# Kernel optimization log

Hardware: AMD Instinct MI355X
Metric: run time of the kernel (lower is better)

Reference implementation:

```python
import jax, jax.numpy as jnp
import numpy as np

H = 64  # hidden_size
B, T1, T2, T3 = 4096, 512, 256, 128


def setup_inputs() -> dict:
    key = jax.random.key(0)
    ks = jax.random.split(key, 18)
    s = 1.0 / np.sqrt(H)  # torch LSTMCell init scale
    def p(k, shape, scale):
        return jax.random.normal(k, shape, dtype=jnp.float32) * scale
    return {
        "x1": p(ks[0], (B, T1), 1.0),
        "x2": p(ks[1], (B, T2), 1.0),
        "x3": p(ks[2], (B, T3), 1.0),
        "W_ih3": p(ks[3], (4 * H, 3), s), "W_hh3": p(ks[4], (4 * H, H), s),
        "b_ih3": p(ks[5], (4 * H,), s), "b_hh3": p(ks[6], (4 * H,), s),
        "W_ih2": p(ks[7], (4 * H, 2), s), "W_hh2": p(ks[8], (4 * H, H), s),
        "b_ih2": p(ks[9], (4 * H,), s), "b_hh2": p(ks[10], (4 * H,), s),
        "W_ih1": p(ks[11], (4 * H, 1), s), "W_hh1": p(ks[12], (4 * H, H), s),
        "b_ih1": p(ks[13], (4 * H,), s), "b_hh1": p(ks[14], (4 * H,), s),
        "W_out": p(ks[15], (1, H), s), "b_out": p(ks[16], (1,), s),
    }


def reference(x1, x2, x3,
              W_ih3, W_hh3, b_ih3, b_hh3,
              W_ih2, W_hh2, b_ih2, b_hh2,
              W_ih1, W_hh1, b_ih1, b_hh1,
              W_out, b_out):
    h = W_hh3.shape[1]
    Bb, t1 = x1.shape
    r2, r3 = t1 // x2.shape[1], t1 // x3.shape[1]
    # Pad input weights to width 3; concat order is [x1, x2, x3] (zeros where absent),
    # so padded-column zeros reproduce the narrower cells exactly.
    Wi = jnp.stack([W_ih3,
                    jnp.pad(W_ih2, ((0, 0), (0, 1))),
                    jnp.pad(W_ih1, ((0, 0), (0, 2)))])  # [3, 4H, 3]
    Wh = jnp.stack([W_hh3, W_hh2, W_hh1])               # [3, 4H, H]
    bs = jnp.stack([b_ih3 + b_hh3, b_ih2 + b_hh2, b_ih1 + b_hh1])  # [3, 4H]
    t = np.arange(t1)
    has2 = (t % r2 == 0)
    has3 = (t % r3 == 0)
    assert not np.any(has3 & ~has2), "ratio2 must divide ratio3 for the concat-order mapping"
    # width 3 -> cell3 (type 0), width 2 -> cell2 (type 1), width 1 -> cell1 (type 2)
    step_type = jnp.asarray(2 - has2.astype(np.int32) - has3.astype(np.int32))
    xs = jnp.zeros((t1, Bb, 3), x1.dtype)
    xs = xs.at[:, :, 0].set(x1.T)
    xs = xs.at[::r2, :, 1].set(x2.T)
    xs = xs.at[::r3, :, 2].set(x3.T)

    def step(carry, inp):
        hx, cx = carry
        x, ty = inp
        g = x @ Wi[ty].T + hx @ Wh[ty].T + bs[ty]  # [B, 4H]
        i, f, gg, o = jnp.split(g, 4, axis=-1)     # torch gate order i,f,g,o
        cx = jax.nn.sigmoid(f) * cx + jax.nn.sigmoid(i) * jnp.tanh(gg)
        hx = jax.nn.sigmoid(o) * jnp.tanh(cx)
        return (hx, cx), None

    z = jnp.zeros((Bb, h), x1.dtype)
    (hx, _), _ = jax.lax.scan(step, (z, z), (xs, step_type))
    return jax.nn.sigmoid(hx @ W_out.T + b_out)  # [B, 1]
```

## Files before the change

### kernel.cpp

```cpp
#include <hip/hip_runtime.h>


typedef __attribute__((ext_vector_type(8))) short short8v;
typedef __attribute__((ext_vector_type(4))) float float4v;
typedef __attribute__((ext_vector_type(2))) float float2v;
typedef __attribute__((ext_vector_type(4))) unsigned int uint4v;
typedef __attribute__((ext_vector_type(2))) unsigned int uint2v;

template <int N> struct IC { static constexpr int value = N; };

#define AST 72

#if __has_builtin(__builtin_amdgcn_exp2f)
#define EXP2F(x) __builtin_amdgcn_exp2f(x)
#else
#define EXP2F(x) exp2f(x)
#endif
#if __has_builtin(__builtin_amdgcn_rcpf)
#define RCPF(x) __builtin_amdgcn_rcpf(x)
#else
#define RCPF(x) (1.0f / (x))
#endif

#define NL2E -1.4426950408889634f
#define NL2E2 -2.8853900817779268f

__device__ __forceinline__ short f2bf(float f) {
  union { float f; unsigned u; } v; v.f = f;
  unsigned r = v.u + 0x7FFFu + ((v.u >> 16) & 1u);
  return (short)(r >> 16);
}
__device__ __forceinline__ float bf2f(short h) {
  union { float f; unsigned u; } v;
  v.u = ((unsigned)(unsigned short)h) << 16;
  return v.f;
}
__device__ __forceinline__ unsigned cvt_pk_bf16(float lo, float hi) {
  unsigned r;
  asm("v_cvt_pk_bf16_f32 %0, %1, %2" : "=v"(r) : "v"(lo), "v"(hi));
  return r;
}
__device__ __forceinline__ unsigned permb(unsigned hi, unsigned lo, unsigned sel) {
#if __has_builtin(__builtin_amdgcn_perm)
  return __builtin_amdgcn_perm(hi, lo, sel);
#else
  union { unsigned u[2]; unsigned char b[8]; } s;
  s.u[0] = lo; s.u[1] = hi;
  unsigned r = 0;
  for (int i = 0; i < 4; ++i) r |= (unsigned)s.b[(sel >> (8 * i)) & 7] << (8 * i);
  return r;
#endif
}
__device__ __forceinline__ float rcp1p(float y) {
  return RCPF(1.0f + EXP2F(y));
}
__device__ __forceinline__ float fsig(float x) { return rcp1p(x * NL2E); }

__global__ __launch_bounds__(256, 1) void mlstm_kernel(
    const float* __restrict__ x1, const float* __restrict__ x2,
    const float* __restrict__ x3,
    const float* __restrict__ Wi3, const float* __restrict__ Wh3,
    const float* __restrict__ bi3, const float* __restrict__ bh3,
    const float* __restrict__ Wi2, const float* __restrict__ Wh2,
    const float* __restrict__ bi2, const float* __restrict__ bh2,
    const float* __restrict__ Wi1, const float* __restrict__ Wh1,
    const float* __restrict__ bi1, const float* __restrict__ bh1,
    const float* __restrict__ Wout, const float* __restrict__ bout,
    float* __restrict__ out) {
  __shared__ __attribute__((aligned(16))) short Ab0[16 * AST];
  __shared__ __attribute__((aligned(16))) short Ab1[16 * AST];

  const int tid = threadIdx.x;
  const int w = tid >> 6;
  const int lane = tid & 63;
  const int q = lane >> 4;
  const int c = lane & 15;
  const int R0 = blockIdx.x << 4;

  for (int idx = tid; idx < 16 * AST; idx += 256) {
    Ab0[idx] = 0;
    Ab1[idx] = 0;
  }

  const float* xr1 = x1 + (size_t)(R0 + c) * 512;
  const float* xr2 = x2 + (size_t)(R0 + c) * 256;
  const float* xr3 = x3 + (size_t)(R0 + c) * 128;

  float4v xf1 = *(const float4v*)(xr1);
  float2v xf2 = *(const float2v*)(xr2);
  float xf3 = xr3[0];

  short8v whs[3][4][2];
  short8v wix[3][4];
  float4v bias4[3][4];
  {
    const float* WhA[3] = {Wh3, Wh2, Wh1};
    const float* WiA[3] = {Wi3, Wi2, Wi1};
    const float* biA[3] = {bi3, bi2, bi1};
    const float* bhA[3] = {bh3, bh2, bh1};
    const int wdt[3] = {3, 2, 1};
#pragma unroll
    for (int ty = 0; ty < 3; ++ty) {
#pragma unroll
      for (int g = 0; g < 4; ++g) {
        const float sg = (g == 2) ? NL2E2 : NL2E;
        const int n = g * 64 + 16 * w + c;
#pragma unroll
        for (int kf = 0; kf < 2; ++kf) {
          short8v v;
#pragma unroll
          for (int j = 0; j < 8; ++j)
            v[j] = f2bf(sg * WhA[ty][n * 64 + kf * 32 + q * 8 + j]);
          whs[ty][g][kf] = v;
        }
        short8v v2 = {0, 0, 0, 0, 0, 0, 0, 0};
        if (q == 0) {
#pragma unroll
          for (int j = 0; j < 3; ++j)
            if (j < wdt[ty]) v2[j] = f2bf(sg * WiA[ty][n * wdt[ty] + j]);
        }
        wix[ty][g] = v2;
        float4v bv;
#pragma unroll
        for (int r = 0; r < 4; ++r) {
          const int nd = g * 64 + 16 * w + 4 * q + r;
          bv[r] = sg * (biA[ty][nd] + bhA[ty][nd]);
        }
        bias4[ty][g] = bv;
      }
    }
  }

  const int afo = c * AST + q * 8;
  const int hwo = c * AST + 16 * w + 4 * q;

  __syncthreads();

  float cx[4] = {0.f, 0.f, 0.f, 0.f};

  unsigned d0, d1, d2, d3, xcw;
  auto cvtgrp = [&]() {
    unsigned pA = cvt_pk_bf16(xf1[0], xf1[1]);
    unsigned pB = cvt_pk_bf16(xf1[2], xf1[3]);
    unsigned p2 = cvt_pk_bf16(xf2[0], xf2[1]);
    xcw = cvt_pk_bf16(xf3, 0.0f);
    d0 = permb(p2, pA, 0x05040100);
    d1 = permb(p2, pA, 0x05040302);
    d2 = permb(p2, pB, 0x07060100);
    d3 = permb(p2, pB, 0x07060302);
  };
  cvtgrp();

  auto stepf = [&](auto tyc, unsigned dS, unsigned dx3, const short* rbuf,
                   short* wbuf) {
    constexpr int TY = decltype(tyc)::value;
    uint4v au = {dS, dx3, 0u, 0u};
    short8v a2 = __builtin_bit_cast(short8v, au);
    short8v a0 = *(const short8v*)(rbuf + afo);
    short8v a1 = *(const short8v*)(rbuf + afo + 32);

    float4v acc[4];
#pragma unroll
    for (int g = 0; g < 4; ++g) {
      float4v z = bias4[TY][g];
      z = __builtin_amdgcn_mfma_f32_16x16x32_bf16(wix[TY][g], a2, z, 0, 0, 0);
      z = __builtin_amdgcn_mfma_f32_16x16x32_bf16(whs[TY][g][0], a0, z, 0, 0, 0);
      z = __builtin_amdgcn_mfma_f32_16x16x32_bf16(whs[TY][g][1], a1, z, 0, 0, 0);
      acc[g] = z;
    }

    float h[4];
#pragma unroll
    for (int r = 0; r < 4; ++r) {
      float e0 = EXP2F(acc[0][r]);
      float e1 = EXP2F(acc[1][r]);
      float e2 = EXP2F(__builtin_fminf(acc[2][r], 60.0f));
      float e3 = EXP2F(acc[3][r]);
      float sitg = (1.0f - e2) * RCPF((1.0f + e0) * (1.0f + e2));
      float ncx = __builtin_fmaf(RCPF(1.0f + e1), cx[r], sitg);
      cx[r] = ncx;
      float e4 = EXP2F(__builtin_fminf(ncx * NL2E2, 60.0f));
      h[r] = (1.0f - e4) * RCPF((1.0f + e3) * (1.0f + e4));
    }
    uint2v pk;
    pk[0] = cvt_pk_bf16(h[0], h[1]);
    pk[1] = cvt_pk_bf16(h[2], h[3]);
    *(uint2v*)(wbuf + hwo) = pk;
    __syncthreads();
  };

  for (int t4 = 0; t4 < 512; t4 += 4) {
    stepf(IC<0>{}, d0, xcw, Ab0, Ab1);
    int tp = (t4 + 4 > 508) ? 508 : (t4 + 4);
    xf1 = *(const float4v*)(xr1 + tp);
    xf2 = *(const float2v*)(xr2 + (tp >> 1));
    xf3 = xr3[tp >> 2];
    stepf(IC<2>{}, d1, xcw, Ab1, Ab0);
    stepf(IC<1>{}, d2, xcw, Ab0, Ab1);
    stepf(IC<2>{}, d3, xcw, Ab1, Ab0);
    cvtgrp();
  }

  if (tid < 16) {
    float s = bout[0];
    const short* hr = Ab0 + tid * AST;
#pragma unroll
    for (int k = 0; k < 64; ++k)
      s = __builtin_fmaf(bf2f(hr[k]), Wout[k], s);
    out[R0 + tid] = fsig(s);
  }
}

extern "C" void kernel_launch(void* const* d_in, const int* in_sizes, int n_in,
                              void* d_out, int out_size, void* d_ws,
                              size_t ws_size, hipStream_t stream) {
  const float* x1 = (const float*)d_in[0];
  const float* x2 = (const float*)d_in[1];
  const float* x3 = (const float*)d_in[2];
  const float* Wi3 = (const float*)d_in[3];
  const float* Wh3 = (const float*)d_in[4];
  const float* bi3 = (const float*)d_in[5];
  const float* bh3 = (const float*)d_in[6];
  const float* Wi2 = (const float*)d_in[7];
  const float* Wh2 = (const float*)d_in[8];
  const float* bi2 = (const float*)d_in[9];
  const float* bh2 = (const float*)d_in[10];
  const float* Wi1 = (const float*)d_in[11];
  const float* Wh1 = (const float*)d_in[12];
  const float* bi1 = (const float*)d_in[13];
  const float* bh1 = (const float*)d_in[14];
  const float* Wout = (const float*)d_in[15];
  const float* bout = (const float*)d_in[16];
  float* out = (float*)d_out;

  hipLaunchKernelGGL(mlstm_kernel, dim3(256), dim3(256), 0, stream,
                     x1, x2, x3, Wi3, Wh3, bi3, bh3, Wi2, Wh2, bi2, bh2,
                     Wi1, Wh1, bi1, bh1, Wout, bout, out);
}
```

Before: 347.0 us.

## Preload bf16-packed inputs into LDS and merge cell-update reciprocals

Before the recurrence, each block converts its 16 rows of x1/x2/x3 to packed bf16 and stores them in shared memory. Inside the time loop it then reads them from LDS instead of issuing global loads and doing per-group conversion and permutes. The intent is to remove global-memory latency and conversion ALU from the serial critical path. Separately, the cell-state update folds the two reciprocals into one by working over a common denominator. The cost is about 41 KB more LDS and a longer prologue, and the larger product in the single reciprocal could lose precision or overflow.

New measurement: 299.4 us. 1.16x faster.

```diff
diff --git a/kernel.cpp b/kernel.cpp
--- a/kernel.cpp
+++ b/kernel.cpp
@@ -10,6 +10,8 @@
 template <int N> struct IC { static constexpr int value = N; };
 
 #define AST 72
+#define XSA 516
+#define XSB 129
 
 #if __has_builtin(__builtin_amdgcn_exp2f)
 #define EXP2F(x) __builtin_amdgcn_exp2f(x)
@@ -39,17 +41,6 @@
   unsigned r;
   asm("v_cvt_pk_bf16_f32 %0, %1, %2" : "=v"(r) : "v"(lo), "v"(hi));
   return r;
-}
-__device__ __forceinline__ unsigned permb(unsigned hi, unsigned lo, unsigned sel) {
-#if __has_builtin(__builtin_amdgcn_perm)
-  return __builtin_amdgcn_perm(hi, lo, sel);
-#else
-  union { unsigned u[2]; unsigned char b[8]; } s;
-  s.u[0] = lo; s.u[1] = hi;
-  unsigned r = 0;
-  for (int i = 0; i < 4; ++i) r |= (unsigned)s.b[(sel >> (8 * i)) & 7] << (8 * i);
-  return r;
-#endif
 }
 __device__ __forceinline__ float rcp1p(float y) {
   return RCPF(1.0f + EXP2F(y));
@@ -69,6 +60,8 @@
     float* __restrict__ out) {
   __shared__ __attribute__((aligned(16))) short Ab0[16 * AST];
   __shared__ __attribute__((aligned(16))) short Ab1[16 * AST];
+  __shared__ __attribute__((aligned(16))) unsigned xAf[16 * XSA];
+  __shared__ __attribute__((aligned(16))) unsigned xBf[16 * XSB];
 
   const int tid = threadIdx.x;
   const int w = tid >> 6;
@@ -77,18 +70,21 @@
   const int c = lane & 15;
   const int R0 = blockIdx.x << 4;
 
+  for (int idx = tid; idx < 16 * 256; idx += 256) {
+    int m = idx >> 8, tp = idx & 255;
+    float2v v1 = *(const float2v*)(x1 + (size_t)(R0 + m) * 512 + 2 * tp);
+    float v2 = x2[(size_t)(R0 + m) * 256 + tp];
+    xAf[m * XSA + 2 * tp] = cvt_pk_bf16(v1[0], v2);
+    xAf[m * XSA + 2 * tp + 1] = cvt_pk_bf16(v1[1], v2);
+  }
+  for (int idx = tid; idx < 16 * 128; idx += 256) {
+    int m = idx >> 7, tt = idx & 127;
+    xBf[m * XSB + tt] = cvt_pk_bf16(x3[(size_t)(R0 + m) * 128 + tt], 0.0f);
+  }
   for (int idx = tid; idx < 16 * AST; idx += 256) {
     Ab0[idx] = 0;
     Ab1[idx] = 0;
   }
-
-  const float* xr1 = x1 + (size_t)(R0 + c) * 512;
-  const float* xr2 = x2 + (size_t)(R0 + c) * 256;
-  const float* xr3 = x3 + (size_t)(R0 + c) * 128;
-
-  float4v xf1 = *(const float4v*)(xr1);
-  float2v xf2 = *(const float2v*)(xr2);
-  float xf3 = xr3[0];
 
   short8v whs[3][4][2];
   short8v wix[3][4];
@@ -133,23 +129,12 @@
 
   const int afo = c * AST + q * 8;
   const int hwo = c * AST + 16 * w + 4 * q;
+  const int xao = c * XSA;
+  const int xbo = c * XSB;
 
   __syncthreads();
 
   float cx[4] = {0.f, 0.f, 0.f, 0.f};
-
-  unsigned d0, d1, d2, d3, xcw;
-  auto cvtgrp = [&]() {
-    unsigned pA = cvt_pk_bf16(xf1[0], xf1[1]);
-    unsigned pB = cvt_pk_bf16(xf1[2], xf1[3]);
-    unsigned p2 = cvt_pk_bf16(xf2[0], xf2[1]);
-    xcw = cvt_pk_bf16(xf3, 0.0f);
-    d0 = permb(p2, pA, 0x05040100);
-    d1 = permb(p2, pA, 0x05040302);
-    d2 = permb(p2, pB, 0x07060100);
-    d3 = permb(p2, pB, 0x07060302);
-  };
-  cvtgrp();
 
   auto stepf = [&](auto tyc, unsigned dS, unsigned dx3, const short* rbuf,
                    short* wbuf) {
@@ -176,8 +161,10 @@
       float e1 = EXP2F(acc[1][r]);
       float e2 = EXP2F(__builtin_fminf(acc[2][r], 60.0f));
       float e3 = EXP2F(acc[3][r]);
-      float sitg = (1.0f - e2) * RCPF((1.0f + e0) * (1.0f + e2));
-      float ncx = __builtin_fmaf(RCPF(1.0f + e1), cx[r], sitg);
+      float a = 1.0f + e0, b = 1.0f + e1, g2 = 1.0f + e2;
+      float ag = a * g2;
+      float Rr = RCPF(ag * b);
+      float ncx = (__builtin_fmaf(cx[r], ag, (1.0f - e2) * b)) * Rr;
       cx[r] = ncx;
       float e4 = EXP2F(__builtin_fminf(ncx * NL2E2, 60.0f));
       h[r] = (1.0f - e4) * RCPF((1.0f + e3) * (1.0f + e4));
@@ -189,16 +176,19 @@
     __syncthreads();
   };
 
+  uint4v xd = *(const uint4v*)(xAf + xao);
+  unsigned xw = xBf[xbo];
+
   for (int t4 = 0; t4 < 512; t4 += 4) {
-    stepf(IC<0>{}, d0, xcw, Ab0, Ab1);
+    stepf(IC<0>{}, xd[0], xw, Ab0, Ab1);
     int tp = (t4 + 4 > 508) ? 508 : (t4 + 4);
-    xf1 = *(const float4v*)(xr1 + tp);
-    xf2 = *(const float2v*)(xr2 + (tp >> 1));
-    xf3 = xr3[tp >> 2];
-    stepf(IC<2>{}, d1, xcw, Ab1, Ab0);
-    stepf(IC<1>{}, d2, xcw, Ab0, Ab1);
-    stepf(IC<2>{}, d3, xcw, Ab1, Ab0);
-    cvtgrp();
+    uint4v xdn = *(const uint4v*)(xAf + xao + tp);
+    unsigned xwn = xBf[xbo + (tp >> 2)];
+    stepf(IC<2>{}, xd[1], xw, Ab1, Ab0);
+    stepf(IC<1>{}, xd[2], xw, Ab0, Ab1);
+    stepf(IC<2>{}, xd[3], xw, Ab1, Ab0);
+    xd = xdn;
+    xw = xwn;
   }
 
   if (tid < 16) {
```
